# Kernel tuning notes

Hardware: AMD Instinct MI355X
Metric: run time of the kernel (lower is better)

Reference implementation:

```python
import jax, jax.numpy as jnp
import numpy as np

B, S, H, I, E, K = 4, 2048, 2048, 5632, 8, 2


def setup_inputs() -> dict:
    key = jax.random.key(0)
    k0, k1, k2, k3, k4 = jax.random.split(key, 5)
    std_p = 1.0 / np.sqrt(H)
    return {
        "hidden_states": jax.random.normal(k0, (B, S, H), dtype=jnp.float32),
        "router_w": jax.random.normal(k1, (E, H), dtype=jnp.float32) * 0.02,
        "w_gate": jax.random.normal(k2, (E, H, I), dtype=jnp.float32) * std_p,
        "w_up": jax.random.normal(k3, (E, H, I), dtype=jnp.float32) * std_p,
        "w_down": jax.random.normal(k4, (E, I, H), dtype=jnp.float32) * (1.0 / np.sqrt(I)),
    }


def reference(hidden_states, router_w, w_gate, w_up, w_down):
    b, s, h = hidden_states.shape
    x = hidden_states.reshape(-1, h)                       # [T, H]
    router_logits = x @ router_w.T                          # [T, E]
    routing_weights = jax.nn.softmax(router_logits, axis=-1)
    top_w, top_i = jax.lax.top_k(routing_weights, K)        # [T, K]
    top_w = top_w / jnp.sum(top_w, axis=-1, keepdims=True)  # renormalize over top-k
    # combine[t, e] = sum_k top_w[t, k] * (top_i[t, k] == e)
    combine = jnp.sum(jax.nn.one_hot(top_i, E, dtype=top_w.dtype) * top_w[..., None], axis=1)  # [T, E]
    out = jnp.zeros_like(x)
    for e in range(E):  # small fixed expert count
        # SwiGLU expert MLP: down(silu(gate(x)) * up(x))
        act = jax.nn.silu(x @ w_gate[e]) * (x @ w_up[e])    # [T, I]
        out = out + (act @ w_down[e]) * combine[:, e:e + 1]
    return (out.reshape(b, s, h),
            router_logits.reshape(b, s, E),
            top_i.reshape(b, s, K),
            top_w.reshape(b, s, K))
```

## Files before the change

kernel.cpp:

```cpp
#include <hip/hip_runtime.h>
#include <hip/hip_bf16.h>
#include <stdint.h>

#define NTOK 8192
#define HD   2048
#define ID   5632
#define NE   8
#define NASSIGN (NTOK * 2)
#define MAXT256 (NASSIGN / 256 + NE)

typedef __attribute__((ext_vector_type(8))) short  bf16x8;
typedef __attribute__((ext_vector_type(4))) float  f32x4;
typedef __attribute__((ext_vector_type(8))) unsigned short u16x8;

__device__ __forceinline__ unsigned short f2bf(float f) {
  union { float f; unsigned int u; } c; c.f = f;
  unsigned int lsb = (c.u >> 16) & 1u;
  return (unsigned short)((c.u + 0x7fffu + lsb) >> 16);
}

__device__ __forceinline__ void async16(const void* g, void* l) {
  __builtin_amdgcn_global_load_lds(
      (const __attribute__((address_space(1))) void*)g,
      (__attribute__((address_space(3))) void*)l, 16, 0, 0);
}

__global__ __launch_bounds__(256) void k_router(
    const float* __restrict__ x, const float* __restrict__ rw,
    float* __restrict__ out_logits, float* __restrict__ out_topi,
    float* __restrict__ out_topw,
    int* __restrict__ tk_e, float* __restrict__ tk_w, int* __restrict__ cnts)
{
  const int wid = threadIdx.x >> 6, lane = threadIdx.x & 63;
  const int t = blockIdx.x * 4 + wid;
  const float* xr = x + (size_t)t * HD;
  float acc[NE];
#pragma unroll
  for (int e = 0; e < NE; e++) acc[e] = 0.f;
#pragma unroll
  for (int i = 0; i < 8; i++) {
    const int col = lane * 4 + i * 256;
    const float4 xv = *(const float4*)(xr + col);
#pragma unroll
    for (int e = 0; e < NE; e++) {
      const float4 wv = *(const float4*)(rw + e * HD + col);
      acc[e] += xv.x * wv.x + xv.y * wv.y + xv.z * wv.z + xv.w * wv.w;
    }
  }
#pragma unroll
  for (int e = 0; e < NE; e++)
    for (int o = 32; o >= 1; o >>= 1) acc[e] += __shfl_xor(acc[e], o, 64);

  if (lane == 0) {
    int i1 = 0;
#pragma unroll
    for (int e = 1; e < NE; e++) if (acc[e] > acc[i1]) i1 = e;
    int i2 = (i1 == 0) ? 1 : 0;
#pragma unroll
    for (int e = 0; e < NE; e++) if (e != i1 && acc[e] > acc[i2]) i2 = e;
    float p2 = __expf(acc[i2] - acc[i1]);
    float s  = 1.f + p2;
    float w1 = 1.f / s, w2 = p2 / s;
#pragma unroll
    for (int e = 0; e < NE; e++) out_logits[(size_t)t * NE + e] = acc[e];
    out_topi[t * 2 + 0] = (float)i1; out_topi[t * 2 + 1] = (float)i2;
    out_topw[t * 2 + 0] = w1;        out_topw[t * 2 + 1] = w2;
    tk_e[t * 2 + 0] = i1; tk_e[t * 2 + 1] = i2;
    tk_w[t * 2 + 0] = w1; tk_w[t * 2 + 1] = w2;
    atomicAdd(&cnts[i1], 1); atomicAdd(&cnts[i2], 1);
  }
}

__global__ void k_scan(const int* __restrict__ cnts, int* __restrict__ offs,
                       int* __restrict__ cursor, int* __restrict__ tile_e,
                       int* __restrict__ tile_rt, int* __restrict__ ntiles) {
  if (threadIdx.x == 0) {
    int s = 0, nt = 0;
    for (int e = 0; e < NE; e++) {
      offs[e] = s; cursor[e] = s;
      int ntl = (cnts[e] + 255) >> 8;
      for (int i = 0; i < ntl; i++) { tile_e[nt] = e; tile_rt[nt] = i; nt++; }
      s += cnts[e];
    }
    ntiles[0] = nt;
  }
}

__global__ void k_assign(const int* __restrict__ tk_e, const float* __restrict__ tk_w,
                         int* __restrict__ cursor, int* __restrict__ perm,
                         float* __restrict__ pw) {
  int t = blockIdx.x * 256 + threadIdx.x;
  if (t >= NTOK) return;
#pragma unroll
  for (int k = 0; k < 2; k++) {
    int e = tk_e[t * 2 + k];
    int pos = atomicAdd(&cursor[e], 1);
    perm[pos] = t;
    pw[pos] = tk_w[t * 2 + k];
  }
}

__global__ __launch_bounds__(256) void k_gather(const float* __restrict__ x,
    const int* __restrict__ perm, unsigned short* __restrict__ xg) {
  const int r = blockIdx.x;
  const int tok = perm[r];
  const float* src = x + (size_t)tok * HD;
  unsigned short* dst = xg + (size_t)r * HD;
  const int c = threadIdx.x * 8;
  float4 a = *(const float4*)(src + c);
  float4 b = *(const float4*)(src + c + 4);
  u16x8 o;
  o[0] = f2bf(a.x); o[1] = f2bf(a.y); o[2] = f2bf(a.z); o[3] = f2bf(a.w);
  o[4] = f2bf(b.x); o[5] = f2bf(b.y); o[6] = f2bf(b.z); o[7] = f2bf(b.w);
  *(u16x8*)(dst + c) = o;
}

__global__ __launch_bounds__(256) void k_conv_gu(const float* __restrict__ wg,
    const float* __restrict__ wu, unsigned short* __restrict__ wgT,
    unsigned short* __restrict__ wuT) {
  __shared__ float tl[32][33];
  const int z = blockIdx.z, e = z >> 1;
  const float* in = ((z & 1) ? wu : wg) + (size_t)e * HD * ID;
  unsigned short* out = ((z & 1) ? wuT : wgT) + (size_t)e * (size_t)ID * HD;
  const int tx = threadIdx.x & 31, ty = threadIdx.x >> 5;
  const int c0 = blockIdx.x * 32, r0 = blockIdx.y * 32;
#pragma unroll
  for (int j = 0; j < 4; j++)
    tl[ty + j * 8][tx] = in[(size_t)(r0 + ty + j * 8) * ID + (c0 + tx)];
  __syncthreads();
#pragma unroll
  for (int j = 0; j < 4; j++) {
    int oc = ty + j * 8;
    out[(size_t)(c0 + oc) * HD + (r0 + tx)] = f2bf(tl[tx][oc]);
  }
}

__global__ __launch_bounds__(256) void k_conv_d(const float* __restrict__ wd,
    unsigned short* __restrict__ wdT) {
  __shared__ float tl[32][33];
  const int e = blockIdx.z;
  const float* in = wd + (size_t)e * ID * HD;
  unsigned short* out = wdT + (size_t)e * (size_t)HD * ID;
  const int tx = threadIdx.x & 31, ty = threadIdx.x >> 5;
  const int c0 = blockIdx.x * 32, r0 = blockIdx.y * 32;
#pragma unroll
  for (int j = 0; j < 4; j++)
    tl[ty + j * 8][tx] = in[(size_t)(r0 + ty + j * 8) * HD + (c0 + tx)];
  __syncthreads();
#pragma unroll
  for (int j = 0; j < 4; j++) {
    int oc = ty + j * 8;
    out[(size_t)(c0 + oc) * ID + (r0 + tx)] = f2bf(tl[tx][oc]);
  }
}

#define HBF(b,kh) (((b)*2+(kh))*32768)

__global__ __launch_bounds__(512, 2) void k_gemm_gu256f(
    const unsigned short* __restrict__ A,
    const unsigned short* __restrict__ BgT, const unsigned short* __restrict__ BuT,
    const int* __restrict__ cnts, const int* __restrict__ offs,
    const int* __restrict__ tile_e, const int* __restrict__ tile_rt,
    const int* __restrict__ ntiles, unsigned short* __restrict__ gact)
{
  const int raw = blockIdx.x;
  const int v = (raw & 7) * ((int)gridDim.x >> 3) + (raw >> 3);
  const int ct = v / MAXT256;
  const int ti = v % MAXT256;
  if (ti >= ntiles[0]) return;
  const int e = tile_e[ti], rt = tile_rt[ti];
  const int cnt = cnts[e], off = offs[e];
  const int tid = threadIdx.x;

  __shared__ __align__(16) char smem[131072];

  const unsigned short* Bg = BgT + (size_t)e * (size_t)ID * HD;
  const unsigned short* Bu = BuT + (size_t)e * (size_t)ID * HD;
  const size_t arow0 = (size_t)off + (size_t)rt * 256;
  const size_t bcol0 = (size_t)ct * 128;

  const int r0s = tid >> 2;
  const int c0s = (((tid & 3) ^ ((tid >> 3) & 3)) * 8);

  const int NT = HD / 64, NIT = NT / 2;

  auto STAGE_A = [&](int bb, int kh, int kt) {
    const int kc = kt * 64 + kh * 32;
    async16(A + (arow0 + r0s) * (size_t)HD + kc + c0s, smem + HBF(bb,kh) + tid * 16);
    async16(A + (arow0 + 128 + r0s) * (size_t)HD + kc + c0s, smem + HBF(bb,kh) + 8192 + tid * 16);
  };
  auto STAGE_B = [&](int bb, int kh, int kt) {
    const int kc = kt * 64 + kh * 32;
    async16(Bg + (bcol0 + r0s) * (size_t)HD + kc + c0s, smem + HBF(bb,kh) + 16384 + tid * 16);
    async16(Bu + (bcol0 + r0s) * (size_t)HD + kc + c0s, smem + HBF(bb,kh) + 24576 + tid * 16);
  };

  f32x4 accg[8][2], accu[8][2];
#pragma unroll
  for (int m = 0; m < 8; m++)
#pragma unroll
    for (int n = 0; n < 2; n++) { accg[m][n] = (f32x4)0.f; accu[m][n] = (f32x4)0.f; }

  const int lane = tid & 63, wid = tid >> 6;
  const int wm = wid >> 2, wn = wid & 3;
  const int fr = lane & 15;
  const int slot = ((lane >> 4) ^ ((fr >> 1) & 3));
  const int laddr = (fr << 6) + (slot << 4);

  STAGE_A(0,0,0); STAGE_B(0,0,0); STAGE_A(0,1,0); STAGE_B(0,1,0);
  STAGE_A(1,0,1); STAGE_B(1,0,1);
  asm volatile("s_waitcnt vmcnt(4)" ::: "memory");
  asm volatile("s_barrier" ::: "memory");

  constexpr int SB[8]  = {1,1,0,0,0,0,1,1};
  constexpr int SOP[8] = {0,1,0,1,0,1,0,1};
  constexpr int SKH[8] = {1,1,0,0,1,1,0,0};
  constexpr int SKO[8] = {1,1,2,2,2,2,3,3};

  bf16x8 bgr[2], bur[2];
  for (int i = 0; i < NIT; ++i) {
#pragma unroll
    for (int p = 0; p < 8; ++p) {
      const int b = p >> 2, kh = (p >> 1) & 1, mh = p & 1;
      bf16x8 afr[4];
#pragma unroll
      for (int t = 0; t < 4; t++)
        afr[t] = *(const bf16x8*)(smem + HBF(b,kh) + ((wm*128 + mh*64 + t*16) << 6) + laddr);
      if (mh == 0) {
#pragma unroll
        for (int t = 0; t < 2; t++) {
          bgr[t] = *(const bf16x8*)(smem + HBF(b,kh) + 16384 + ((wn*32 + t*16) << 6) + laddr);
          bur[t] = *(const bf16x8*)(smem + HBF(b,kh) + 24576 + ((wn*32 + t*16) << 6) + laddr);
        }
      }
      {
        int kt = 2 * i + SKO[p]; kt = kt < NT - 1 ? kt : NT - 1;
        if (SOP[p] == 0) STAGE_A(SB[p], SKH[p], kt);
        else             STAGE_B(SB[p], SKH[p], kt);
      }
      asm volatile("s_barrier" ::: "memory");
      __builtin_amdgcn_s_setprio(1);
#pragma unroll
      for (int t = 0; t < 4; t++)
#pragma unroll
        for (int n = 0; n < 2; n++) {
          accg[mh*4 + t][n] = __builtin_amdgcn_mfma_f32_16x16x32_bf16(afr[t], bgr[n], accg[mh*4 + t][n], 0, 0, 0);
          accu[mh*4 + t][n] = __builtin_amdgcn_mfma_f32_16x16x32_bf16(afr[t], bur[n], accu[mh*4 + t][n], 0, 0, 0);
        }
      __builtin_amdgcn_s_setprio(0);
      if (p == 3 || p == 7) asm volatile("s_waitcnt vmcnt(4)" ::: "memory");
      asm volatile("s_barrier" ::: "memory");
    }
  }
  asm volatile("s_waitcnt vmcnt(0)" ::: "memory");

  const int crow = (lane >> 4) * 4, ccol = lane & 15;
  const int rbase = rt * 256 + wm * 128;
#pragma unroll
  for (int mt = 0; mt < 8; ++mt) {
#pragma unroll
    for (int j = 0; j < 4; ++j) {
      const int rl = rbase + mt * 16 + crow + j;
      if (rl >= cnt) continue;
      const size_t grow = (size_t)off + rl;
#pragma unroll
      for (int nt = 0; nt < 2; ++nt) {
        const int col = (int)bcol0 + wn * 32 + nt * 16 + ccol;
        const float g = accg[mt][nt][j], u = accu[mt][nt][j];
        const float a = g / (1.f + __expf(-g)) * u;
        gact[grow * (size_t)ID + col] = f2bf(a);
      }
    }
  }
}

#define HB(b,kh,op) (((((b)*2+(kh))*2)+(op))*16384)

__global__ __launch_bounds__(512, 2) void k_gemm_dn256(
    const unsigned short* __restrict__ A,
    const unsigned short* __restrict__ Wbase,
    const int* __restrict__ cnts, const int* __restrict__ offs,
    const int* __restrict__ tile_e, const int* __restrict__ tile_rt,
    const int* __restrict__ ntiles,
    const int* __restrict__ perm, const float* __restrict__ pw,
    float* __restrict__ out)
{
  const int raw = blockIdx.x;
  const int v = (raw & 7) * ((int)gridDim.x >> 3) + (raw >> 3);
  const int ct = v / MAXT256;
  const int ti = v % MAXT256;
  if (ti >= ntiles[0]) return;
  const int e = tile_e[ti], rt = tile_rt[ti];
  const int cnt = cnts[e], off = offs[e];
  const int tid = threadIdx.x;

  __shared__ __align__(16) char smem[131072];

  const unsigned short* W = Wbase + (size_t)e * (size_t)HD * ID;
  const size_t arow0 = (size_t)off + (size_t)rt * 256;
  const size_t bcol0 = (size_t)ct * 256;

  const int r0s = tid >> 2;
  const int c0s = (((tid & 3) ^ ((tid >> 3) & 3)) * 8);

  const int NT = ID / 64, NIT = NT / 2;

  auto STAGE_A = [&](int bb, int kh, int kt) {
    const int kc = kt * 64 + kh * 32;
    async16(A + (arow0 + r0s) * (size_t)ID + kc + c0s, smem + HB(bb,kh,0) + tid * 16);
    async16(A + (arow0 + 128 + r0s) * (size_t)ID + kc + c0s, smem + HB(bb,kh,0) + 8192 + tid * 16);
  };
  auto STAGE_B = [&](int bb, int kh, int kt) {
    const int kc = kt * 64 + kh * 32;
    async16(W + (bcol0 + r0s) * (size_t)ID + kc + c0s, smem + HB(bb,kh,1) + tid * 16);
    async16(W + (bcol0 + 128 + r0s) * (size_t)ID + kc + c0s, smem + HB(bb,kh,1) + 8192 + tid * 16);
  };

  f32x4 acc[8][4];
#pragma unroll
  for (int m = 0; m < 8; m++)
#pragma unroll
    for (int n = 0; n < 4; n++) acc[m][n] = (f32x4)0.f;

  const int lane = tid & 63, wid = tid >> 6;
  const int wm = wid >> 2, wn = wid & 3;
  const int fr = lane & 15;
  const int slot = ((lane >> 4) ^ ((fr >> 1) & 3));
  const int laddr = (fr << 6) + (slot << 4);

  STAGE_A(0,0,0); STAGE_B(0,0,0); STAGE_A(0,1,0); STAGE_B(0,1,0);
  STAGE_A(1,0,1); STAGE_B(1,0,1);
  asm volatile("s_waitcnt vmcnt(4)" ::: "memory");
  asm volatile("s_barrier" ::: "memory");

  constexpr int SB[8]  = {1,1,0,0,0,0,1,1};
  constexpr int SOP[8] = {0,1,0,1,0,1,0,1};
  constexpr int SKH[8] = {1,1,0,0,1,1,0,0};
  constexpr int SKO[8] = {1,1,2,2,2,2,3,3};

  bf16x8 bfr[4];
  for (int i = 0; i < NIT; ++i) {
#pragma unroll
    for (int p = 0; p < 8; ++p) {
      const int b = p >> 2, kh = (p >> 1) & 1, mh = p & 1;
      bf16x8 afr[4];
#pragma unroll
      for (int t = 0; t < 4; t++)
        afr[t] = *(const bf16x8*)(smem + HB(b,kh,0) + ((wm*128 + mh*64 + t*16) << 6) + laddr);
      if (mh == 0) {
#pragma unroll
        for (int t = 0; t < 4; t++)
          bfr[t] = *(const bf16x8*)(smem + HB(b,kh,1) + ((wn*64 + t*16) << 6) + laddr);
      }
      {
        int kt = 2 * i + SKO[p]; kt = kt < NT - 1 ? kt : NT - 1;
        if (SOP[p] == 0) STAGE_A(SB[p], SKH[p], kt);
        else             STAGE_B(SB[p], SKH[p], kt);
      }
      asm volatile("s_barrier" ::: "memory");
      __builtin_amdgcn_s_setprio(1);
#pragma unroll
      for (int t = 0; t < 4; t++)
#pragma unroll
        for (int n = 0; n < 4; n++)
          acc[mh*4 + t][n] = __builtin_amdgcn_mfma_f32_16x16x32_bf16(afr[t], bfr[n], acc[mh*4 + t][n], 0, 0, 0);
      __builtin_amdgcn_s_setprio(0);
      if (p == 3 || p == 7) asm volatile("s_waitcnt vmcnt(4)" ::: "memory");
      asm volatile("s_barrier" ::: "memory");
    }
  }
  asm volatile("s_waitcnt vmcnt(0)" ::: "memory");

  const int crow = (lane >> 4) * 4, ccol = lane & 15;
  const int rbase = rt * 256 + wm * 128;
#pragma unroll
  for (int mt = 0; mt < 8; ++mt) {
#pragma unroll
    for (int j = 0; j < 4; ++j) {
      const int rl = rbase + mt * 16 + crow + j;
      if (rl >= cnt) continue;
      const size_t grow = (size_t)off + rl;
      const int tok = perm[grow];
      const float wgt = pw[grow];
#pragma unroll
      for (int nt = 0; nt < 4; ++nt) {
        const int col = (int)bcol0 + wn * 64 + nt * 16 + ccol;
        atomicAdd(&out[(size_t)tok * HD + col], acc[mt][nt][j] * wgt);
      }
    }
  }
}

extern "C" void kernel_launch(void* const* d_in, const int* in_sizes, int n_in,
                              void* d_out, int out_size, void* d_ws, size_t ws_size,
                              hipStream_t stream) {
  const float* x  = (const float*)d_in[0];
  const float* rw = (const float*)d_in[1];
  const float* wg = (const float*)d_in[2];
  const float* wu = (const float*)d_in[3];
  const float* wd = (const float*)d_in[4];

  float* outp       = (float*)d_out;
  float* out_logits = outp + (size_t)NTOK * HD;
  float* out_topi   = out_logits + (size_t)NTOK * NE;
  float* out_topw   = out_topi + (size_t)NTOK * 2;

  char* w = (char*)d_ws;
  int*   cnts    = (int*)(w + 0);
  int*   offs    = (int*)(w + 64);
  int*   cursor  = (int*)(w + 128);
  int*   ntiles  = (int*)(w + 192);
  int*   tile_e  = (int*)(w + 256);
  int*   tile_rt = (int*)(w + 1280);
  int*   tk_e    = (int*)(w + 4096);
  float* tk_w    = (float*)(w + 4096 + 65536);
  int*   perm    = (int*)(w + 4096 + 2 * 65536);
  float* pw      = (float*)(w + 4096 + 3 * 65536);

  char* big = w + (1 << 20);
  unsigned short* xg = (unsigned short*)big;
  const size_t XG_E = (size_t)(NASSIGN + 256) * HD;
  unsigned short* wgT = xg + XG_E;
  const size_t WT_E = (size_t)NE * ID * HD;
  unsigned short* wuT  = wgT + WT_E;
  unsigned short* wdT  = wuT + WT_E;
  unsigned short* gact = wdT + WT_E;

  hipMemsetAsync(d_ws, 0, 256, stream);
  hipMemsetAsync(d_out, 0, (size_t)NTOK * HD * sizeof(float), stream);

  k_conv_gu<<<dim3(ID / 32, HD / 32, 2 * NE), 256, 0, stream>>>(wg, wu, wgT, wuT);
  k_conv_d<<<dim3(HD / 32, ID / 32, NE), 256, 0, stream>>>(wd, wdT);

  k_router<<<NTOK / 4, 256, 0, stream>>>(x, rw, out_logits, out_topi, out_topw,
                                         tk_e, tk_w, cnts);
  k_scan<<<1, 64, 0, stream>>>(cnts, offs, cursor, tile_e, tile_rt, ntiles);
  k_assign<<<NTOK / 256, 256, 0, stream>>>(tk_e, tk_w, cursor, perm, pw);
  k_gather<<<NASSIGN, 256, 0, stream>>>(x, perm, xg);

  k_gemm_gu256f<<<dim3((ID / 128) * MAXT256), 512, 0, stream>>>(
      xg, wgT, wuT, cnts, offs, tile_e, tile_rt, ntiles, gact);
  k_gemm_dn256<<<dim3((HD / 256) * MAXT256), 512, 0, stream>>>(
      gact, wdT, cnts, offs, tile_e, tile_rt, ntiles, perm, pw, outp);
}
```

Baseline: 1.935 ms.

## Shrink gate/up GEMM tile to 256x64 with simple double buffer for occupancy

Narrows the gate/up GEMM column tile from 128 to 64 and replaces the eight-phase, two-half-K software pipeline with a plain two-stage double buffer over K steps of 32. This cuts LDS use from 128 KB to 48 KB so launch bounds can ask for four blocks per CU, and it halves the accumulator registers. The cost is lower arithmetic intensity: the A tile is re-read from global memory twice as often, each K step carries less MFMA work between barriers, and the grid doubles in size.

```diff
diff --git a/kernel.cpp b/kernel.cpp
--- a/kernel.cpp
+++ b/kernel.cpp
@@ -154,9 +154,7 @@
   }
 }
 
-#define HBF(b,kh) (((b)*2+(kh))*32768)
-
-__global__ __launch_bounds__(512, 2) void k_gemm_gu256f(
+__global__ __launch_bounds__(512, 4) void k_gemm_gu256f(
     const unsigned short* __restrict__ A,
     const unsigned short* __restrict__ BgT, const unsigned short* __restrict__ BuT,
     const int* __restrict__ cnts, const int* __restrict__ offs,
@@ -172,34 +170,34 @@
   const int cnt = cnts[e], off = offs[e];
   const int tid = threadIdx.x;
 
-  __shared__ __align__(16) char smem[131072];
+  __shared__ __align__(16) char smem[49152];
 
   const unsigned short* Bg = BgT + (size_t)e * (size_t)ID * HD;
   const unsigned short* Bu = BuT + (size_t)e * (size_t)ID * HD;
   const size_t arow0 = (size_t)off + (size_t)rt * 256;
-  const size_t bcol0 = (size_t)ct * 128;
+  const size_t bcol0 = (size_t)ct * 64;
 
   const int r0s = tid >> 2;
   const int c0s = (((tid & 3) ^ ((tid >> 3) & 3)) * 8);
-
-  const int NT = HD / 64, NIT = NT / 2;
-
-  auto STAGE_A = [&](int bb, int kh, int kt) {
-    const int kc = kt * 64 + kh * 32;
-    async16(A + (arow0 + r0s) * (size_t)HD + kc + c0s, smem + HBF(bb,kh) + tid * 16);
-    async16(A + (arow0 + 128 + r0s) * (size_t)HD + kc + c0s, smem + HBF(bb,kh) + 8192 + tid * 16);
+  const int ub  = tid & 255;
+  const int rbs = ub >> 2;
+  const int cbs = (((ub & 3) ^ ((ub >> 3) & 3)) * 8);
+  const unsigned short* Bsrc = (tid < 256) ? Bg : Bu;
+  const int bdst = (tid < 256) ? 16384 : 20480;
+
+  const int NT = HD / 32;
+
+  auto STAGE = [&](int bb, int kt) {
+    const int kc = kt * 32;
+    char* base = smem + bb * 24576;
+    async16(A + (arow0 + r0s) * (size_t)HD + kc + c0s, base + tid * 16);
+    async16(A + (arow0 + 128 + r0s) * (size_t)HD + kc + c0s, base + 8192 + tid * 16);
+    async16(Bsrc + (bcol0 + rbs) * (size_t)HD + kc + cbs, base + bdst + ub * 16);
   };
-  auto STAGE_B = [&](int bb, int kh, int kt) {
-    const int kc = kt * 64 + kh * 32;
-    async16(Bg + (bcol0 + r0s) * (size_t)HD + kc + c0s, smem + HBF(bb,kh) + 16384 + tid * 16);
-    async16(Bu + (bcol0 + r0s) * (size_t)HD + kc + c0s, smem + HBF(bb,kh) + 24576 + tid * 16);
-  };
-
-  f32x4 accg[8][2], accu[8][2];
-#pragma unroll
-  for (int m = 0; m < 8; m++)
-#pragma unroll
-    for (int n = 0; n < 2; n++) { accg[m][n] = (f32x4)0.f; accu[m][n] = (f32x4)0.f; }
+
+  f32x4 accg[8], accu[8];
+#pragma unroll
+  for (int m = 0; m < 8; m++) { accg[m] = (f32x4)0.f; accu[m] = (f32x4)0.f; }
 
   const int lane = tid & 63, wid = tid >> 6;
   const int wm = wid >> 2, wn = wid & 3;
@@ -207,50 +205,27 @@
   const int slot = ((lane >> 4) ^ ((fr >> 1) & 3));
   const int laddr = (fr << 6) + (slot << 4);
 
-  STAGE_A(0,0,0); STAGE_B(0,0,0); STAGE_A(0,1,0); STAGE_B(0,1,0);
-  STAGE_A(1,0,1); STAGE_B(1,0,1);
-  asm volatile("s_waitcnt vmcnt(4)" ::: "memory");
-  asm volatile("s_barrier" ::: "memory");
-
-  constexpr int SB[8]  = {1,1,0,0,0,0,1,1};
-  constexpr int SOP[8] = {0,1,0,1,0,1,0,1};
-  constexpr int SKH[8] = {1,1,0,0,1,1,0,0};
-  constexpr int SKO[8] = {1,1,2,2,2,2,3,3};
-
-  bf16x8 bgr[2], bur[2];
-  for (int i = 0; i < NIT; ++i) {
-#pragma unroll
-    for (int p = 0; p < 8; ++p) {
-      const int b = p >> 2, kh = (p >> 1) & 1, mh = p & 1;
-      bf16x8 afr[4];
-#pragma unroll
-      for (int t = 0; t < 4; t++)
-        afr[t] = *(const bf16x8*)(smem + HBF(b,kh) + ((wm*128 + mh*64 + t*16) << 6) + laddr);
-      if (mh == 0) {
-#pragma unroll
-        for (int t = 0; t < 2; t++) {
-          bgr[t] = *(const bf16x8*)(smem + HBF(b,kh) + 16384 + ((wn*32 + t*16) << 6) + laddr);
-          bur[t] = *(const bf16x8*)(smem + HBF(b,kh) + 24576 + ((wn*32 + t*16) << 6) + laddr);
-        }
-      }
-      {
-        int kt = 2 * i + SKO[p]; kt = kt < NT - 1 ? kt : NT - 1;
-        if (SOP[p] == 0) STAGE_A(SB[p], SKH[p], kt);
-        else             STAGE_B(SB[p], SKH[p], kt);
-      }
-      asm volatile("s_barrier" ::: "memory");
-      __builtin_amdgcn_s_setprio(1);
-#pragma unroll
-      for (int t = 0; t < 4; t++)
-#pragma unroll
-        for (int n = 0; n < 2; n++) {
-          accg[mh*4 + t][n] = __builtin_amdgcn_mfma_f32_16x16x32_bf16(afr[t], bgr[n], accg[mh*4 + t][n], 0, 0, 0);
-          accu[mh*4 + t][n] = __builtin_amdgcn_mfma_f32_16x16x32_bf16(afr[t], bur[n], accu[mh*4 + t][n], 0, 0, 0);
-        }
-      __builtin_amdgcn_s_setprio(0);
-      if (p == 3 || p == 7) asm volatile("s_waitcnt vmcnt(4)" ::: "memory");
-      asm volatile("s_barrier" ::: "memory");
-    }
+  STAGE(0, 0);
+  int cur = 0;
+  for (int kt = 0; kt < NT; ++kt) {
+    const int nk = (kt + 1 < NT) ? kt + 1 : NT - 1;
+    STAGE(cur ^ 1, nk);
+    asm volatile("s_waitcnt vmcnt(3)" ::: "memory");
+    asm volatile("s_barrier" ::: "memory");
+    char* base = smem + cur * 24576;
+    bf16x8 bgr = *(const bf16x8*)(base + 16384 + ((wn * 16) << 6) + laddr);
+    bf16x8 bur = *(const bf16x8*)(base + 20480 + ((wn * 16) << 6) + laddr);
+    __builtin_amdgcn_s_setprio(1);
+#pragma unroll
+    for (int mt = 0; mt < 8; ++mt) {
+      bf16x8 afr = *(const bf16x8*)(base + ((wm * 128 + mt * 16) << 6) + laddr);
+      accg[mt] = __builtin_amdgcn_mfma_f32_16x16x32_bf16(afr, bgr, accg[mt], 0, 0, 0);
+      accu[mt] = __builtin_amdgcn_mfma_f32_16x16x32_bf16(afr, bur, accu[mt], 0, 0, 0);
+    }
+    __builtin_amdgcn_s_setprio(0);
+    asm volatile("s_waitcnt lgkmcnt(0)" ::: "memory");
+    asm volatile("s_barrier" ::: "memory");
+    cur ^= 1;
   }
   asm volatile("s_waitcnt vmcnt(0)" ::: "memory");
 
@@ -263,13 +238,10 @@
       const int rl = rbase + mt * 16 + crow + j;
       if (rl >= cnt) continue;
       const size_t grow = (size_t)off + rl;
-#pragma unroll
-      for (int nt = 0; nt < 2; ++nt) {
-        const int col = (int)bcol0 + wn * 32 + nt * 16 + ccol;
-        const float g = accg[mt][nt][j], u = accu[mt][nt][j];
-        const float a = g / (1.f + __expf(-g)) * u;
-        gact[grow * (size_t)ID + col] = f2bf(a);
-      }
+      const int col = (int)bcol0 + wn * 16 + ccol;
+      const float g = accg[mt][j], u = accu[mt][j];
+      const float a = g / (1.f + __expf(-g)) * u;
+      gact[grow * (size_t)ID + col] = f2bf(a);
     }
   }
 }
@@ -438,7 +410,7 @@
   k_assign<<<NTOK / 256, 256, 0, stream>>>(tk_e, tk_w, cursor, perm, pw);
   k_gather<<<NASSIGN, 256, 0, stream>>>(x, perm, xg);
 
-  k_gemm_gu256f<<<dim3((ID / 128) * MAXT256), 512, 0, stream>>>(
+  k_gemm_gu256f<<<dim3((ID / 64) * MAXT256), 512, 0, stream>>>(
       xg, wgT, wuT, cnts, offs, tile_e, tile_rt, ntiles, gact);
   k_gemm_dn256<<<dim3((HD / 256) * MAXT256), 512, 0, stream>>>(
       gact, wdT, cnts, offs, tile_e, tile_rt, ntiles, perm, pw, outp);
```

Result: slower. 2.132 ms (+10.2%).

## Replace atomic scatter with per-assignment buffer plus combine; widen weight transpose tiles

Applied to the files above, without the earlier changes.

The down-projection GEMM now writes each weighted assignment row into a dense fp32 staging buffer instead of doing scattered float atomicAdds into the output. A new combine kernel uses an inverse permutation recorded in k_assign to sum each token's two expert rows, so the output memset is no longer needed. The weight transpose/convert kernels are merged into one 64x64-tile kernel that converts to bf16 before the shared-memory transpose and writes 16-byte vectors. The trade-off is an extra kernel launch and roughly 128 MB of fp32 staging traffic in place of the atomics.

```diff
diff --git a/kernel.cpp b/kernel.cpp
--- a/kernel.cpp
+++ b/kernel.cpp
@@ -88,7 +88,7 @@
 
 __global__ void k_assign(const int* __restrict__ tk_e, const float* __restrict__ tk_w,
                          int* __restrict__ cursor, int* __restrict__ perm,
-                         float* __restrict__ pw) {
+                         float* __restrict__ pw, int* __restrict__ inv) {
   int t = blockIdx.x * 256 + threadIdx.x;
   if (t >= NTOK) return;
 #pragma unroll
@@ -97,6 +97,7 @@
     int pos = atomicAdd(&cursor[e], 1);
     perm[pos] = t;
     pw[pos] = tk_w[t * 2 + k];
+    inv[t * 2 + k] = pos;
   }
 }
 
@@ -115,42 +116,31 @@
   *(u16x8*)(dst + c) = o;
 }
 
-__global__ __launch_bounds__(256) void k_conv_gu(const float* __restrict__ wg,
-    const float* __restrict__ wu, unsigned short* __restrict__ wgT,
-    unsigned short* __restrict__ wuT) {
-  __shared__ float tl[32][33];
-  const int z = blockIdx.z, e = z >> 1;
-  const float* in = ((z & 1) ? wu : wg) + (size_t)e * HD * ID;
-  unsigned short* out = ((z & 1) ? wuT : wgT) + (size_t)e * (size_t)ID * HD;
-  const int tx = threadIdx.x & 31, ty = threadIdx.x >> 5;
-  const int c0 = blockIdx.x * 32, r0 = blockIdx.y * 32;
-#pragma unroll
-  for (int j = 0; j < 4; j++)
-    tl[ty + j * 8][tx] = in[(size_t)(r0 + ty + j * 8) * ID + (c0 + tx)];
+__global__ __launch_bounds__(256) void k_conv64(const float* __restrict__ in0,
+    const float* __restrict__ in1, unsigned short* __restrict__ out0,
+    unsigned short* __restrict__ out1, int R, int C, int nmat) {
+  __shared__ unsigned short tlb[64][72];
+  const int z = blockIdx.z;
+  const int mat = (nmat == 2) ? (z & 1) : 0;
+  const int e   = (nmat == 2) ? (z >> 1) : z;
+  const float* in = ((mat == 0) ? in0 : in1) + (size_t)e * R * C;
+  unsigned short* out = ((mat == 0) ? out0 : out1) + (size_t)e * (size_t)R * C;
+  const int tid = threadIdx.x;
+  const int c0 = blockIdx.x * 64, r0 = blockIdx.y * 64;
+#pragma unroll
+  for (int pass = 0; pass < 4; ++pass) {
+    const int kr = pass * 16 + (tid >> 4);
+    const int cc = (tid & 15) * 4;
+    const float4 v = *(const float4*)(in + (size_t)(r0 + kr) * C + c0 + cc);
+    tlb[cc + 0][kr] = f2bf(v.x); tlb[cc + 1][kr] = f2bf(v.y);
+    tlb[cc + 2][kr] = f2bf(v.z); tlb[cc + 3][kr] = f2bf(v.w);
+  }
   __syncthreads();
 #pragma unroll
-  for (int j = 0; j < 4; j++) {
-    int oc = ty + j * 8;
-    out[(size_t)(c0 + oc) * HD + (r0 + tx)] = f2bf(tl[tx][oc]);
-  }
-}
-
-__global__ __launch_bounds__(256) void k_conv_d(const float* __restrict__ wd,
-    unsigned short* __restrict__ wdT) {
-  __shared__ float tl[32][33];
-  const int e = blockIdx.z;
-  const float* in = wd + (size_t)e * ID * HD;
-  unsigned short* out = wdT + (size_t)e * (size_t)HD * ID;
-  const int tx = threadIdx.x & 31, ty = threadIdx.x >> 5;
-  const int c0 = blockIdx.x * 32, r0 = blockIdx.y * 32;
-#pragma unroll
-  for (int j = 0; j < 4; j++)
-    tl[ty + j * 8][tx] = in[(size_t)(r0 + ty + j * 8) * HD + (c0 + tx)];
-  __syncthreads();
-#pragma unroll
-  for (int j = 0; j < 4; j++) {
-    int oc = ty + j * 8;
-    out[(size_t)(c0 + oc) * ID + (r0 + tx)] = f2bf(tl[tx][oc]);
+  for (int pass = 0; pass < 2; ++pass) {
+    const int n = pass * 32 + (tid >> 3);
+    const int k = (tid & 7) * 8;
+    *(u16x8*)(out + (size_t)(c0 + n) * R + r0 + k) = *(const u16x8*)&tlb[n][k];
   }
 }
 
@@ -282,8 +272,7 @@
     const int* __restrict__ cnts, const int* __restrict__ offs,
     const int* __restrict__ tile_e, const int* __restrict__ tile_rt,
     const int* __restrict__ ntiles,
-    const int* __restrict__ perm, const float* __restrict__ pw,
-    float* __restrict__ out)
+    const float* __restrict__ pw, float* __restrict__ dbuf)
 {
   const int raw = blockIdx.x;
   const int v = (raw & 7) * ((int)gridDim.x >> 3) + (raw >> 3);
@@ -380,14 +369,28 @@
       const int rl = rbase + mt * 16 + crow + j;
       if (rl >= cnt) continue;
       const size_t grow = (size_t)off + rl;
-      const int tok = perm[grow];
       const float wgt = pw[grow];
 #pragma unroll
       for (int nt = 0; nt < 4; ++nt) {
         const int col = (int)bcol0 + wn * 64 + nt * 16 + ccol;
-        atomicAdd(&out[(size_t)tok * HD + col], acc[mt][nt][j] * wgt);
-      }
-    }
+        dbuf[grow * (size_t)HD + col] = acc[mt][nt][j] * wgt;
+      }
+    }
+  }
+}
+
+__global__ __launch_bounds__(256) void k_combine(const float* __restrict__ dbuf,
+    const int* __restrict__ inv, float* __restrict__ out) {
+  const int t = blockIdx.x;
+  const int p0 = inv[t * 2], p1 = inv[t * 2 + 1];
+  const float4* r0 = (const float4*)(dbuf + (size_t)p0 * HD);
+  const float4* r1 = (const float4*)(dbuf + (size_t)p1 * HD);
+  float4* o = (float4*)(out + (size_t)t * HD);
+#pragma unroll
+  for (int i = 0; i < 2; i++) {
+    int c = threadIdx.x + i * 256;
+    float4 a = r0[c], b = r1[c];
+    o[c] = make_float4(a.x + b.x, a.y + b.y, a.z + b.z, a.w + b.w);
   }
 }
 
@@ -416,6 +419,7 @@
   float* tk_w    = (float*)(w + 4096 + 65536);
   int*   perm    = (int*)(w + 4096 + 2 * 65536);
   float* pw      = (float*)(w + 4096 + 3 * 65536);
+  int*   inv     = (int*)(w + 4096 + 4 * 65536);
 
   char* big = w + (1 << 20);
   unsigned short* xg = (unsigned short*)big;
@@ -425,21 +429,25 @@
   unsigned short* wuT  = wgT + WT_E;
   unsigned short* wdT  = wuT + WT_E;
   unsigned short* gact = wdT + WT_E;
+  const size_t GA_E = (size_t)(NASSIGN + 256) * ID;
+  float* dbuf = (float*)(gact + GA_E);
 
   hipMemsetAsync(d_ws, 0, 256, stream);
-  hipMemsetAsync(d_out, 0, (size_t)NTOK * HD * sizeof(float), stream);
-
-  k_conv_gu<<<dim3(ID / 32, HD / 32, 2 * NE), 256, 0, stream>>>(wg, wu, wgT, wuT);
-  k_conv_d<<<dim3(HD / 32, ID / 32, NE), 256, 0, stream>>>(wd, wdT);
+
+  k_conv64<<<dim3(ID / 64, HD / 64, 2 * NE), 256, 0, stream>>>(
+      wg, wu, wgT, wuT, HD, ID, 2);
+  k_conv64<<<dim3(HD / 64, ID / 64, NE), 256, 0, stream>>>(
+      wd, nullptr, wdT, nullptr, ID, HD, 1);
 
   k_router<<<NTOK / 4, 256, 0, stream>>>(x, rw, out_logits, out_topi, out_topw,
                                          tk_e, tk_w, cnts);
   k_scan<<<1, 64, 0, stream>>>(cnts, offs, cursor, tile_e, tile_rt, ntiles);
-  k_assign<<<NTOK / 256, 256, 0, stream>>>(tk_e, tk_w, cursor, perm, pw);
+  k_assign<<<NTOK / 256, 256, 0, stream>>>(tk_e, tk_w, cursor, perm, pw, inv);
   k_gather<<<NASSIGN, 256, 0, stream>>>(x, perm, xg);
 
   k_gemm_gu256f<<<dim3((ID / 128) * MAXT256), 512, 0, stream>>>(
       xg, wgT, wuT, cnts, offs, tile_e, tile_rt, ntiles, gact);
   k_gemm_dn256<<<dim3((HD / 256) * MAXT256), 512, 0, stream>>>(
-      gact, wdT, cnts, offs, tile_e, tile_rt, ntiles, perm, pw, outp);
-}
+      gact, wdT, cnts, offs, tile_e, tile_rt, ntiles, pw, dbuf);
+  k_combine<<<NTOK, 256, 0, stream>>>(dbuf, inv, outp);
+}
```

Result: faster. 1.855 ms (-4.2%).
